# Performance work log

Measured on AMD Instinct MI355X. Metric: run time of the kernel, lower is better.

## Reference

```python
import jax, jax.numpy as jnp
import numpy as np

HIDDEN = 4096
N_HEADS = 32
N_KV_HEADS = 8
HEAD_DIM = 128
ROPE_THETA = 10000.0


def setup_inputs() -> dict:
    key = jax.random.key(0)
    ks = jax.random.split(key, 6)
    B, S = 1, 2048
    hidden_states = jax.random.normal(ks[0], (B, S, HIDDEN), dtype=jnp.float32)
    position_ids = jnp.arange(S, dtype=jnp.int64 if jax.config.jax_enable_x64 else jnp.int32)[None, :].astype(jnp.int32)
    scale = 0.02
    Wq = jax.random.normal(ks[1], (HIDDEN, N_HEADS * HEAD_DIM), dtype=jnp.float32) * scale
    Wk = jax.random.normal(ks[2], (HIDDEN, N_KV_HEADS * HEAD_DIM), dtype=jnp.float32) * scale
    Wv = jax.random.normal(ks[3], (HIDDEN, N_KV_HEADS * HEAD_DIM), dtype=jnp.float32) * scale
    Wo = jax.random.normal(ks[4], (N_HEADS * HEAD_DIM, HIDDEN), dtype=jnp.float32) * scale
    return {"hidden_states": hidden_states, "position_ids": position_ids,
            "Wq": Wq, "Wk": Wk, "Wv": Wv, "Wo": Wo}


def _rope_cos_sin(position_ids):
    # neox-style rope over full head_dim (rotary_dim == head_dim)
    half = HEAD_DIM // 2
    inv_freq = 1.0 / (ROPE_THETA ** (jnp.arange(0, half, dtype=jnp.float32) / half))
    angles = position_ids.astype(jnp.float32)[..., None] * inv_freq  # [B, S, half]
    return jnp.cos(angles), jnp.sin(angles)


def _apply_rope(x, cos, sin):
    # x: [B, S, H, D]; cos/sin: [B, S, D/2] broadcast over heads
    x1, x2 = jnp.split(x, 2, axis=-1)
    c = cos[:, :, None, :]
    s = sin[:, :, None, :]
    return jnp.concatenate([x1 * c - x2 * s, x2 * c + x1 * s], axis=-1)


def reference(hidden_states, position_ids, Wq, Wk, Wv, Wo):
    B, S, _ = hidden_states.shape
    q = hidden_states @ Wq  # [B, S, H*D]
    k = hidden_states @ Wk  # [B, S, Hkv*D]
    v = hidden_states @ Wv
    q = q.reshape(B, S, N_HEADS, HEAD_DIM)
    k = k.reshape(B, S, N_KV_HEADS, HEAD_DIM)
    v = v.reshape(B, S, N_KV_HEADS, HEAD_DIM)
    cos, sin = _rope_cos_sin(position_ids)
    q = _apply_rope(q, cos, sin)
    k = _apply_rope(k, cos, sin)
    # GQA: expand kv heads to match query heads
    rep = N_HEADS // N_KV_HEADS
    k = jnp.repeat(k, rep, axis=2)  # [B, S, H, D]
    v = jnp.repeat(v, rep, axis=2)
    scale = 1.0 / jnp.sqrt(jnp.asarray(HEAD_DIM, dtype=q.dtype))
    scores = jnp.einsum('bqhd,bkhd->bhqk', q, k) * scale  # [B, H, S, S]
    causal = jnp.tril(jnp.ones((S, S), dtype=bool))
    scores = jnp.where(causal[None, None], scores, jnp.asarray(-1e30, dtype=scores.dtype))
    probs = jax.nn.softmax(scores, axis=-1)
    attn = jnp.einsum('bhqk,bkhd->bqhd', probs, v)  # [B, S, H, D]
    attn = attn.reshape(B, S, N_HEADS * HEAD_DIM)
    return attn @ Wo  # [B, S, HIDDEN]
```

## Files before the change

### kernel.cpp

```cpp
#include <hip/hip_runtime.h>
#include <hip/hip_bf16.h>
#include <math.h>

#define HIDDEN 4096
#define NH 32
#define NKV 8
#define HD 128
#define QKVC 6144

using f32x4  = __attribute__((ext_vector_type(4))) float;
using frag_ab = __attribute__((ext_vector_type(8))) short;

__device__ __forceinline__ short f2bf(float x){
  __hip_bfloat16 h = __float2bfloat16(x);
  return *reinterpret_cast<short*>(&h);
}
__device__ __forceinline__ float bf2f(short s){
  __hip_bfloat16 h = *reinterpret_cast<__hip_bfloat16*>(&s);
  return __bfloat162float(h);
}

__device__ __forceinline__ void load_lds16(const void* g, void* l){
  __builtin_amdgcn_global_load_lds(
      (const __attribute__((address_space(1))) unsigned*)g,
      (__attribute__((address_space(3))) unsigned*)l, 16, 0, 0);
}

__global__ __launch_bounds__(256) void k_cvt(const float* __restrict__ X, short* __restrict__ Y, int n4){
  int i = blockIdx.x*256 + threadIdx.x;
  if (i >= n4) return;
  float4 v = reinterpret_cast<const float4*>(X)[i];
  short4 o;
  o.x = f2bf(v.x); o.y = f2bf(v.y); o.z = f2bf(v.z); o.w = f2bf(v.w);
  reinterpret_cast<short4*>(Y)[i] = o;
}

__global__ __launch_bounds__(256) void k_transpose(const float* __restrict__ W, short* __restrict__ WT,
                                                   int K, int N){
  __shared__ float tile[32][33];
  int n0 = blockIdx.x*32, k0 = blockIdx.y*32;
  int tx = threadIdx.x & 31, ty = threadIdx.x >> 5;
  #pragma unroll
  for (int i=0;i<4;i++) tile[ty+i*8][tx] = W[(size_t)(k0+ty+i*8)*N + n0+tx];
  __syncthreads();
  #pragma unroll
  for (int i=0;i<4;i++) WT[(size_t)(n0+ty+i*8)*K + k0+tx] = f2bf(tile[tx][ty+i*8]);
}

__global__ __launch_bounds__(256) void k_transpose_v(const short* __restrict__ QKV, short* __restrict__ VT){
  __shared__ short tile[32][40];
  int s0 = blockIdx.x*32, d0 = blockIdx.y*32;
  int tx = threadIdx.x & 31, ty = threadIdx.x >> 5;
  #pragma unroll
  for (int i=0;i<4;i++) tile[ty+i*8][tx] = QKV[(size_t)(s0+ty+i*8)*QKVC + 5120 + d0+tx];
  __syncthreads();
  #pragma unroll
  for (int i=0;i<4;i++) VT[(size_t)(d0+ty+i*8)*2048 + s0+tx] = tile[tx][ty+i*8];
}

template<typename OutT>
__global__ __launch_bounds__(256) void k_gemm_bt(const short* __restrict__ A, const short* __restrict__ BT,
                                                 OutT* __restrict__ C, int M, int N, int K){
  __shared__ __align__(16) short As[128*64];
  __shared__ __align__(16) short Bs[128*64];
  const int brow = blockIdx.x*128, bcol = blockIdx.y*128;
  const int t = threadIdx.x, lane = t & 63, wid = t >> 6;
  const int wm = wid >> 1, wn = wid & 1;
  const int l15 = lane & 15, lg = lane >> 4;
  f32x4 acc[4][4] = {};
  const int nk = K >> 6;
  for (int kt = 0; kt < nk; ++kt){
    __syncthreads();
    #pragma unroll
    for (int i=0;i<4;i++){
      int slot = t + i*256;
      int row  = slot >> 3;
      int col  = (slot & 7) << 3;
      load_lds16(A  + (size_t)(brow+row)*K + (size_t)kt*64 + col, &As[slot*8]);
      load_lds16(BT + (size_t)(bcol+row)*K + (size_t)kt*64 + col, &Bs[slot*8]);
    }
    __syncthreads();
    #pragma unroll
    for (int ks=0; ks<2; ++ks){
      frag_ab a[4], b[4];
      #pragma unroll
      for (int mi=0;mi<4;mi++) a[mi] = *(const frag_ab*)&As[(wm*64+mi*16+l15)*64 + ks*32 + lg*8];
      #pragma unroll
      for (int ni=0;ni<4;ni++) b[ni] = *(const frag_ab*)&Bs[(wn*64+ni*16+l15)*64 + ks*32 + lg*8];
      #pragma unroll
      for (int mi=0;mi<4;mi++)
        #pragma unroll
        for (int ni=0;ni<4;ni++)
          acc[mi][ni] = __builtin_amdgcn_mfma_f32_16x16x32_bf16(a[mi], b[ni], acc[mi][ni], 0, 0, 0);
    }
  }
  #pragma unroll
  for (int mi=0;mi<4;mi++)
    #pragma unroll
    for (int ni=0;ni<4;ni++)
      #pragma unroll
      for (int r=0;r<4;r++){
        size_t row = brow + wm*64 + mi*16 + lg*4 + r;
        size_t col = bcol + wn*64 + ni*16 + l15;
        float v = acc[mi][ni][r];
        if constexpr (sizeof(OutT) == 4) C[row*(size_t)N + col] = v;
        else                             C[row*(size_t)N + col] = f2bf(v);
      }
}

__global__ __launch_bounds__(256) void k_rope(short* __restrict__ QKV, const int* __restrict__ pos){
  int idx = blockIdx.x*256 + threadIdx.x;
  int j   = idx & 63;
  int hh  = (idx >> 6) % 40;
  int row = (idx >> 6) / 40;
  int colbase = hh < NH ? hh*HD : HIDDEN + (hh-NH)*HD;
  size_t base = (size_t)row*QKVC + colbase;
  float x1 = bf2f(QKV[base + j]), x2 = bf2f(QKV[base + j + 64]);
  float ang = (float)pos[row] * exp2f(-(float)j * 0.2076205059304601f);
  float sn, cs; sincosf(ang, &sn, &cs);
  QKV[base + j]      = f2bf(x1*cs - x2*sn);
  QKV[base + j + 64] = f2bf(x2*cs + x1*sn);
}

__global__ __launch_bounds__(256) void k_attn(const short* __restrict__ QKV, const short* __restrict__ VT,
                                              short* __restrict__ Attn){
  const int pairI = blockIdx.x, h = blockIdx.y, kvh = h >> 2;
  const int t = threadIdx.x, lane = t & 63, w = t >> 6;
  const int l15 = lane & 15, lg = lane >> 4;
  __shared__ __align__(16) short Ks[32*128];
  __shared__ __align__(16) short Vs[128*40];
  __shared__ __align__(16) short Ps[4][16*40];

  const float SC = 0.08838834764831845f;

  for (int half = 0; half < 2; ++half){
    const int qt = half ? (31 - pairI) : pairI;
    frag_ab aq[4];
    {
      const short* qrow = QKV + (size_t)(qt*64 + w*16 + l15)*QKVC + h*HD;
      #pragma unroll
      for (int ks=0;ks<4;ks++) aq[ks] = *(const frag_ab*)&qrow[ks*32 + lg*8];
    }
    float mrow[4], lrow[4];
    #pragma unroll
    for (int r=0;r<4;r++){ mrow[r] = -INFINITY; lrow[r] = 0.f; }
    f32x4 o[8] = {};
    const int nkv = 2*qt + 2;
    for (int kt = 0; kt < nkv; ++kt){
      __syncthreads();
      #pragma unroll
      for (int i=0;i<2;i++){
        int s = t + i*256;
        int row = s >> 4;
        int c8  = (s & 15) << 3;
        int csw = c8 ^ ((row & 7) << 3);
        load_lds16(QKV + (size_t)(kt*32 + row)*QKVC + HIDDEN + kvh*HD + csw, &Ks[s*8]);
      }
      #pragma unroll
      for (int i=0;i<2;i++){
        int s = t + i*256;
        int d  = s >> 2;
        int k8 = (s & 3) << 3;
        uint4 vv = *(const uint4*)&VT[(size_t)(kvh*HD + d)*2048 + kt*32 + k8];
        *(uint4*)&Vs[d*40 + k8] = vv;
      }
      __syncthreads();
      f32x4 sc[2] = {};
      #pragma unroll
      for (int ks=0;ks<4;ks++){
        int c = ks*32 + lg*8;
        frag_ab b0 = *(const frag_ab*)&Ks[l15*128      + (c ^ ((l15 & 7) << 3))];
        frag_ab b1 = *(const frag_ab*)&Ks[(16+l15)*128 + (c ^ ((l15 & 7) << 3))];
        sc[0] = __builtin_amdgcn_mfma_f32_16x16x32_bf16(aq[ks], b0, sc[0], 0, 0, 0);
        sc[1] = __builtin_amdgcn_mfma_f32_16x16x32_bf16(aq[ks], b1, sc[1], 0, 0, 0);
      }
      float p0[4], p1[4];
      #pragma unroll
      for (int r=0;r<4;r++){
        int rowg = qt*64 + w*16 + lg*4 + r;
        int c0 = kt*32 + l15, c1 = c0 + 16;
        float v0 = sc[0][r]*SC, v1 = sc[1][r]*SC;
        if (c0 > rowg) v0 = -1e30f;
        if (c1 > rowg) v1 = -1e30f;
        float pm = fmaxf(v0, v1);
        pm = fmaxf(pm, __shfl_xor(pm, 1));
        pm = fmaxf(pm, __shfl_xor(pm, 2));
        pm = fmaxf(pm, __shfl_xor(pm, 4));
        pm = fmaxf(pm, __shfl_xor(pm, 8));
        float mn = fmaxf(mrow[r], pm);
        float f  = __expf(mrow[r] - mn);
        mrow[r] = mn;
        float e0 = __expf(v0 - mn), e1 = __expf(v1 - mn);
        float ps = e0 + e1;
        ps += __shfl_xor(ps, 1); ps += __shfl_xor(ps, 2);
        ps += __shfl_xor(ps, 4); ps += __shfl_xor(ps, 8);
        lrow[r] = lrow[r]*f + ps;
        p0[r] = e0; p1[r] = e1;
        #pragma unroll
        for (int df=0;df<8;df++) o[df][r] *= f;
      }
      #pragma unroll
      for (int r=0;r<4;r++){
        Ps[w][(lg*4+r)*40 + l15]      = f2bf(p0[r]);
        Ps[w][(lg*4+r)*40 + 16 + l15] = f2bf(p1[r]);
      }
      frag_ab pa = *(const frag_ab*)&Ps[w][l15*40 + lg*8];
      #pragma unroll
      for (int df=0;df<8;df++){
        frag_ab vb = *(const frag_ab*)&Vs[(df*16+l15)*40 + lg*8];
        o[df] = __builtin_amdgcn_mfma_f32_16x16x32_bf16(pa, vb, o[df], 0, 0, 0);
      }
    }
    #pragma unroll
    for (int df=0;df<8;df++)
      #pragma unroll
      for (int r=0;r<4;r++){
        size_t row = qt*64 + w*16 + lg*4 + r;
        size_t col = (size_t)h*HD + df*16 + l15;
        Attn[row*HIDDEN + col] = f2bf(o[df][r] / lrow[r]);
      }
  }
}

extern "C" void kernel_launch(void* const* d_in, const int* in_sizes, int n_in,
                              void* d_out, int out_size, void* d_ws, size_t ws_size,
                              hipStream_t stream) {
  const float* H  = (const float*)d_in[0];
  const int*  pos = (const int*)  d_in[1];
  const float* Wq = (const float*)d_in[2];
  const float* Wk = (const float*)d_in[3];
  const float* Wv = (const float*)d_in[4];
  const float* Wo = (const float*)d_in[5];
  float* out = (float*)d_out;

  char* ws = (char*)d_ws;
  short* WT   = (short*)(ws);
  short* WoT  = (short*)(ws + 50331648);
  short* Hb   = (short*)(ws + 83886080);
  short* QKV  = (short*)(ws + 100663296);
  short* Attn = (short*)(ws + 125829120);
  short* VT   = Hb;

  k_cvt<<<8192, 256, 0, stream>>>(H, Hb, 2097152);
  k_transpose<<<dim3(128,128), 256, 0, stream>>>(Wq, WT,                        4096, 4096);
  k_transpose<<<dim3( 32,128), 256, 0, stream>>>(Wk, WT + (size_t)4096*4096,    4096, 1024);
  k_transpose<<<dim3( 32,128), 256, 0, stream>>>(Wv, WT + (size_t)5120*4096,    4096, 1024);
  k_transpose<<<dim3(128,128), 256, 0, stream>>>(Wo, WoT,                       4096, 4096);

  k_gemm_bt<short><<<dim3(16,48), 256, 0, stream>>>(Hb, WT, QKV, 2048, 6144, 4096);
  k_rope<<<20480, 256, 0, stream>>>(QKV, pos);
  k_transpose_v<<<dim3(64,32), 256, 0, stream>>>(QKV, VT);
  k_attn<<<dim3(16,32), 256, 0, stream>>>(QKV, VT, Attn);
  k_gemm_bt<float><<<dim3(16,32), 256, 0, stream>>>(Attn, WoT, out, 2048, 4096, 4096);
}
```

Before: 629.7 us.

## Replace GEMM with 256x128-tile, 4-stage LDS-pipelined, XCD-swizzled kernel

Replaces the single-buffered 128x128 GEMM with a 512-thread kernel computing 256x128 tiles over K-steps of 32. A 4-deep ring of LDS buffers with explicit vmcnt waits overlaps global-to-LDS loads with MFMA work, and s_setprio raises priority around the MFMA burst. Block IDs are swizzled across the 8 XCDs for cache locality. The aim is to hide memory latency and cut barrier stalls in the QKV and output projections, at the cost of hand-tuned waitcnt logic that depends on how many loads are in flight.

```diff
diff --git a/kernel.cpp b/kernel.cpp
--- a/kernel.cpp
+++ b/kernel.cpp
@@ -24,6 +24,12 @@
   __builtin_amdgcn_global_load_lds(
       (const __attribute__((address_space(1))) unsigned*)g,
       (__attribute__((address_space(3))) unsigned*)l, 16, 0, 0);
+}
+
+__device__ __forceinline__ void hard_barrier(){
+  asm volatile("" ::: "memory");
+  __builtin_amdgcn_s_barrier();
+  asm volatile("" ::: "memory");
 }
 
 __global__ __launch_bounds__(256) void k_cvt(const float* __restrict__ X, short* __restrict__ Y, int n4){
@@ -59,50 +65,72 @@
 }
 
 template<typename OutT>
-__global__ __launch_bounds__(256) void k_gemm_bt(const short* __restrict__ A, const short* __restrict__ BT,
-                                                 OutT* __restrict__ C, int M, int N, int K){
-  __shared__ __align__(16) short As[128*64];
-  __shared__ __align__(16) short Bs[128*64];
-  const int brow = blockIdx.x*128, bcol = blockIdx.y*128;
-  const int t = threadIdx.x, lane = t & 63, wid = t >> 6;
-  const int wm = wid >> 1, wn = wid & 1;
+__global__ __launch_bounds__(512, 2) void k_gemm256(const short* __restrict__ A, const short* __restrict__ BT,
+                                                    OutT* __restrict__ C, int M, int N, int K, int mt){
+  __shared__ __align__(16) short L[49152];
+  const int nwg = gridDim.x, cpx = nwg >> 3;
+  const int bid = blockIdx.x;
+  const int swz = (bid & 7) * cpx + (bid >> 3);
+  const int bx = swz % mt, by = swz / mt;
+  const int brow = bx*256, bcol = by*128;
+  const int tid = threadIdx.x, lane = tid & 63, wid = tid >> 6;
+  const int wr = wid >> 1, wc = wid & 1;
   const int l15 = lane & 15, lg = lane >> 4;
+  const int nk = K >> 5;
+
+  const int ca0r = tid >> 2,        ca0c = (tid & 3) << 3;
+  const int ca1r = (tid+512) >> 2,  ca1c = ((tid+512) & 3) << 3;
+  const int cbr  = tid >> 2,        cbc  = (tid & 3) << 3;
+  const short* Aponly = A + (size_t)brow*K;
+  const short* Bponly = BT + (size_t)bcol*K;
+
   f32x4 acc[4][4] = {};
-  const int nk = K >> 6;
-  for (int kt = 0; kt < nk; ++kt){
-    __syncthreads();
-    #pragma unroll
-    for (int i=0;i<4;i++){
-      int slot = t + i*256;
-      int row  = slot >> 3;
-      int col  = (slot & 7) << 3;
-      load_lds16(A  + (size_t)(brow+row)*K + (size_t)kt*64 + col, &As[slot*8]);
-      load_lds16(BT + (size_t)(bcol+row)*K + (size_t)kt*64 + col, &Bs[slot*8]);
-    }
-    __syncthreads();
-    #pragma unroll
-    for (int ks=0; ks<2; ++ks){
-      frag_ab a[4], b[4];
-      #pragma unroll
-      for (int mi=0;mi<4;mi++) a[mi] = *(const frag_ab*)&As[(wm*64+mi*16+l15)*64 + ks*32 + lg*8];
-      #pragma unroll
-      for (int ni=0;ni<4;ni++) b[ni] = *(const frag_ab*)&Bs[(wn*64+ni*16+l15)*64 + ks*32 + lg*8];
-      #pragma unroll
-      for (int mi=0;mi<4;mi++)
-        #pragma unroll
-        for (int ni=0;ni<4;ni++)
-          acc[mi][ni] = __builtin_amdgcn_mfma_f32_16x16x32_bf16(a[mi], b[ni], acc[mi][ni], 0, 0, 0);
-    }
+
+  #define STAGE(kt) do { \
+    int _b = (kt) & 3; \
+    load_lds16(Aponly + (size_t)ca0r*K + (kt)*32 + ca0c, &L[_b*12288 + tid*8]); \
+    load_lds16(Aponly + (size_t)ca1r*K + (kt)*32 + ca1c, &L[_b*12288 + (tid+512)*8]); \
+    load_lds16(Bponly + (size_t)cbr*K + (kt)*32 + cbc,  &L[_b*12288 + 8192 + tid*8]); \
+  } while(0)
+
+  STAGE(0); STAGE(1); STAGE(2);
+  asm volatile("s_waitcnt vmcnt(6)" ::: "memory");
+  hard_barrier();
+
+  for (int t = 0; t < nk; ++t){
+    const int b = t & 3;
+    const short* Ab = &L[b*12288];
+    const short* Bb = &L[b*12288 + 8192];
+    frag_ab af[4], bf[4];
+    #pragma unroll
+    for (int m=0;m<4;m++) af[m] = *(const frag_ab*)&Ab[(wr*64 + m*16 + l15)*32 + lg*8];
+    #pragma unroll
+    for (int n=0;n<4;n++) bf[n] = *(const frag_ab*)&Bb[(wc*64 + n*16 + l15)*32 + lg*8];
+    if (t + 3 < nk) STAGE(t+3);
+    hard_barrier();
+    __builtin_amdgcn_s_setprio(1);
+    #pragma unroll
+    for (int m=0;m<4;m++)
+      #pragma unroll
+      for (int n=0;n<4;n++)
+        acc[m][n] = __builtin_amdgcn_mfma_f32_16x16x32_bf16(af[m], bf[n], acc[m][n], 0, 0, 0);
+    __builtin_amdgcn_s_setprio(0);
+    if (t < nk-3)       asm volatile("s_waitcnt vmcnt(6)" ::: "memory");
+    else if (t == nk-3) asm volatile("s_waitcnt vmcnt(3)" ::: "memory");
+    else                asm volatile("s_waitcnt vmcnt(0)" ::: "memory");
+    hard_barrier();
   }
-  #pragma unroll
-  for (int mi=0;mi<4;mi++)
-    #pragma unroll
-    for (int ni=0;ni<4;ni++)
-      #pragma unroll
-      for (int r=0;r<4;r++){
-        size_t row = brow + wm*64 + mi*16 + lg*4 + r;
-        size_t col = bcol + wn*64 + ni*16 + l15;
-        float v = acc[mi][ni][r];
+  #undef STAGE
+
+  #pragma unroll
+  for (int m=0;m<4;m++)
+    #pragma unroll
+    for (int n=0;n<4;n++)
+      #pragma unroll
+      for (int r=0;r<4;r++){
+        size_t row = brow + wr*64 + m*16 + lg*4 + r;
+        size_t col = bcol + wc*64 + n*16 + l15;
+        float v = acc[m][n][r];
         if constexpr (sizeof(OutT) == 4) C[row*(size_t)N + col] = v;
         else                             C[row*(size_t)N + col] = f2bf(v);
       }
@@ -247,9 +275,9 @@
   k_transpose<<<dim3( 32,128), 256, 0, stream>>>(Wv, WT + (size_t)5120*4096,    4096, 1024);
   k_transpose<<<dim3(128,128), 256, 0, stream>>>(Wo, WoT,                       4096, 4096);
 
-  k_gemm_bt<short><<<dim3(16,48), 256, 0, stream>>>(Hb, WT, QKV, 2048, 6144, 4096);
+  k_gemm256<short><<<384, 512, 0, stream>>>(Hb, WT, QKV, 2048, 6144, 4096, 8);
   k_rope<<<20480, 256, 0, stream>>>(QKV, pos);
   k_transpose_v<<<dim3(64,32), 256, 0, stream>>>(QKV, VT);
   k_attn<<<dim3(16,32), 256, 0, stream>>>(QKV, VT, Attn);
-  k_gemm_bt<float><<<dim3(16,32), 256, 0, stream>>>(Attn, WoT, out, 2048, 4096, 4096);
-}
+  k_gemm256<float><<<256, 512, 0, stream>>>(Attn, WoT, out, 2048, 4096, 4096, 8);
+}
```

Measured after the change: 595.3 us. 5.5% less time.
